# Kernel tuning notes

Measured on AMD Instinct MI355X. Metric: run time of the kernel, lower is better.

The kernel has to match this reference:

```python
import jax, jax.numpy as jnp
import numpy as np

HID, HEADS, EXP = 1024, 16, 4
HEAD_DIM = HID // HEADS
EPS = 1e-5


def setup_inputs() -> dict:
    key = jax.random.key(0)
    ks = jax.random.split(key, 16)
    s = 1.0 / np.sqrt(HID)
    d = dict(
        x=jax.random.normal(ks[0], (4, 2048, HID), jnp.float32),
        norm1_g=jnp.ones((HID,), jnp.float32),
        norm1_b=jnp.zeros((HID,), jnp.float32),
        wq=jax.random.normal(ks[1], (HID, HID), jnp.float32) * s,
        bq=jnp.zeros((HID,), jnp.float32),
        wk=jax.random.normal(ks[2], (HID, HID), jnp.float32) * s,
        bk=jnp.zeros((HID,), jnp.float32),
        wv=jax.random.normal(ks[3], (HID, HID), jnp.float32) * s,
        bv=jnp.zeros((HID,), jnp.float32),
        wo=jax.random.normal(ks[4], (HID, HID), jnp.float32) * s,
        bo=jnp.zeros((HID,), jnp.float32),
        norm2_g=jnp.ones((HID,), jnp.float32),
        norm2_b=jnp.zeros((HID,), jnp.float32),
        w1=jax.random.normal(ks[5], (HID * EXP, HID), jnp.float32) * s,
        b1=jnp.zeros((HID * EXP,), jnp.float32),
        w2=jax.random.normal(ks[6], (HID, HID * EXP), jnp.float32) * (1.0 / np.sqrt(HID * EXP)),
        b2=jnp.zeros((HID,), jnp.float32),
    )
    return d


def _layernorm(x, g, b):
    mu = jnp.mean(x, axis=-1, keepdims=True)
    var = jnp.mean(jnp.square(x - mu), axis=-1, keepdims=True)
    return (x - mu) * jax.lax.rsqrt(var + EPS) * g + b


def reference(x, norm1_g, norm1_b, wq, bq, wk, bk, wv, bv, wo, bo,
              norm2_g, norm2_b, w1, b1, w2, b2):
    B, S, _ = x.shape
    h = _layernorm(x, norm1_g, norm1_b)
    q = (h @ wq.T + bq).reshape(B, S, HEADS, HEAD_DIM)
    k = (h @ wk.T + bk).reshape(B, S, HEADS, HEAD_DIM)
    v = (h @ wv.T + bv).reshape(B, S, HEADS, HEAD_DIM)
    # scores: [B, H, S, S] (materialized, matching the naive original)
    scores = jnp.einsum('bshd,bthd->bhst', q, k) / np.sqrt(HEAD_DIM)
    attn = jax.nn.softmax(scores, axis=-1)
    out = jnp.einsum('bhst,bthd->bshd', attn, v).reshape(B, S, HID)
    x = x + out @ wo.T + bo
    h = _layernorm(x, norm2_g, norm2_b)
    ffn = jax.nn.relu(h @ w1.T + b1) @ w2.T + b2
    return x + ffn
```

## Files before the change

kernel.cpp:

```cpp
#include <hip/hip_runtime.h>
#include <hip/hip_bf16.h>

#define HID   1024
#define S_LEN 2048
#define NB    4
#define M_TOK 8192
#define HEADS 16
#define DH    64
#define FFN   4096

typedef __attribute__((ext_vector_type(8))) __bf16 bf16x8;
typedef __attribute__((ext_vector_type(4))) __bf16 bf16x4;
typedef __attribute__((ext_vector_type(4))) float  f32x4;

__device__ __forceinline__ void gl_lds16(const void* g, void* l) {
  __builtin_amdgcn_global_load_lds(
      (const __attribute__((address_space(1))) void*)g,
      (__attribute__((address_space(3))) void*)l, 16, 0, 0);
}

__device__ __forceinline__ int k3f(int r) { return (r ^ (r >> 3)) & 7; }

__global__ __launch_bounds__(256)
void cast_all_kernel(const float* __restrict__ a, const float* __restrict__ b,
                     const float* __restrict__ c, const float* __restrict__ d,
                     const float* __restrict__ e, const float* __restrict__ f,
                     __bf16* __restrict__ oa, __bf16* __restrict__ ob,
                     __bf16* __restrict__ oc, __bf16* __restrict__ od,
                     __bf16* __restrict__ oe, __bf16* __restrict__ og) {
  const int blk = blockIdx.x;
  const float* src; __bf16* dst; int boff;
  if (blk < 4096) {
    const int r = blk >> 10;
    src = (r == 0) ? a : (r == 1) ? b : (r == 2) ? c : d;
    dst = (r == 0) ? oa : (r == 1) ? ob : (r == 2) ? oc : od;
    boff = blk & 1023;
  } else if (blk < 8192) { src = e; dst = oe; boff = blk - 4096; }
  else                   { src = f; dst = og; boff = blk - 8192; }
  const int i = boff * 256 + threadIdx.x;
  float4 v = reinterpret_cast<const float4*>(src)[i];
  bf16x4 o = { (__bf16)v.x, (__bf16)v.y, (__bf16)v.z, (__bf16)v.w };
  reinterpret_cast<bf16x4*>(dst)[i] = o;
}

__global__ __launch_bounds__(256)
void ln_kernel(const float* __restrict__ x, const float* __restrict__ g,
               const float* __restrict__ bb, __bf16* __restrict__ out) {
  const int row = blockIdx.x;
  const int tid = threadIdx.x;
  const float4 v = reinterpret_cast<const float4*>(x + (size_t)row * HID)[tid];
  float s  = v.x + v.y + v.z + v.w;
  float sq = v.x*v.x + v.y*v.y + v.z*v.z + v.w*v.w;
  #pragma unroll
  for (int o = 32; o > 0; o >>= 1) { s += __shfl_down(s, o); sq += __shfl_down(sq, o); }
  __shared__ float ls[4], lq[4];
  if ((tid & 63) == 0) { ls[tid >> 6] = s; lq[tid >> 6] = sq; }
  __syncthreads();
  s  = ls[0] + ls[1] + ls[2] + ls[3];
  sq = lq[0] + lq[1] + lq[2] + lq[3];
  const float mu   = s * (1.0f / HID);
  const float rstd = rsqrtf(sq * (1.0f / HID) - mu * mu + 1e-5f);
  const float4 gv = reinterpret_cast<const float4*>(g)[tid];
  const float4 bv = reinterpret_cast<const float4*>(bb)[tid];
  bf16x4 o;
  o[0] = (__bf16)((v.x - mu) * rstd * gv.x + bv.x);
  o[1] = (__bf16)((v.y - mu) * rstd * gv.y + bv.y);
  o[2] = (__bf16)((v.z - mu) * rstd * gv.z + bv.z);
  o[3] = (__bf16)((v.w - mu) * rstd * gv.w + bv.w);
  reinterpret_cast<bf16x4*>(out + (size_t)row * HID)[tid] = o;
}

template<int EPI>
__global__ __launch_bounds__(256)
void gemm_bt(const __bf16* __restrict__ A, const __bf16* __restrict__ Bw,
             const float* __restrict__ bias, const float* __restrict__ res,
             __bf16* __restrict__ obf, float* __restrict__ of,
             int M, int N, int K) {
  __shared__ __bf16 Al[128 * 64];
  __shared__ __bf16 Bl[128 * 64];
  const int tid  = threadIdx.x;
  const int lane = tid & 63;
  const int wid  = tid >> 6;
  const int wm = wid >> 1, wn = wid & 1;
  const int nwg = gridDim.x * gridDim.y;
  const int bid = blockIdx.y * gridDim.x + blockIdx.x;
  const int swz = (bid & 7) * (nwg >> 3) + (bid >> 3);
  const long bm = (long)(swz / gridDim.x) * 128;
  const long bn = (long)(swz % gridDim.x) * 128;
  const int r8 = lane >> 3, c8 = lane & 7;

  f32x4 acc[4][4] = {};

  const int nk = K >> 6;
  for (int kt = 0; kt < nk; ++kt) {
    const int k0 = kt << 6;
    __syncthreads();
    #pragma unroll
    for (int i = 0; i < 4; ++i) {
      const int rbase = i * 32 + wid * 8;
      gl_lds16(A + (bm + rbase + r8) * (long)K + k0 + c8 * 8, &Al[rbase * 64]);
    }
    #pragma unroll
    for (int i = 0; i < 4; ++i) {
      const int rbase = i * 32 + wid * 8;
      gl_lds16(Bw + (bn + rbase + r8) * (long)K + k0 + c8 * 8, &Bl[rbase * 64]);
    }
    __syncthreads();
    #pragma unroll
    for (int kk = 0; kk < 2; ++kk) {
      bf16x8 af[4], bfr[4];
      #pragma unroll
      for (int mt = 0; mt < 4; ++mt)
        af[mt] = *(const bf16x8*)&Al[(wm * 64 + mt * 16 + (lane & 15)) * 64 + kk * 32 + (lane >> 4) * 8];
      #pragma unroll
      for (int nt = 0; nt < 4; ++nt)
        bfr[nt] = *(const bf16x8*)&Bl[(wn * 64 + nt * 16 + (lane & 15)) * 64 + kk * 32 + (lane >> 4) * 8];
      #pragma unroll
      for (int mt = 0; mt < 4; ++mt)
        #pragma unroll
        for (int nt = 0; nt < 4; ++nt)
          acc[mt][nt] = __builtin_amdgcn_mfma_f32_16x16x32_bf16(af[mt], bfr[nt], acc[mt][nt], 0, 0, 0);
    }
  }

  #pragma unroll
  for (int mt = 0; mt < 4; ++mt) {
    const long row0 = bm + wm * 64 + mt * 16 + ((lane >> 4) << 2);
    #pragma unroll
    for (int nt = 0; nt < 4; ++nt) {
      const long col = bn + wn * 64 + nt * 16 + (lane & 15);
      const float bsv = bias[col];
      #pragma unroll
      for (int j = 0; j < 4; ++j) {
        const float val = acc[mt][nt][j] + bsv;
        const long idx = (row0 + j) * (long)N + col;
        if (EPI == 2) of[idx] = res[idx] + val;
        else          obf[idx] = (__bf16)val;
      }
    }
  }
}

template<int EPI>
__global__ __launch_bounds__(512, 2)
void gemm_bt256(const __bf16* __restrict__ A, const __bf16* __restrict__ Bw,
                const float* __restrict__ bias,
                __bf16* __restrict__ obf, __bf16* __restrict__ ob2,
                __bf16* __restrict__ ob3, int M, int N, int K) {
  __shared__ __bf16 Al[2][256 * 64];
  __shared__ __bf16 Bl[2][256 * 64];
  const int tid  = threadIdx.x;
  const int lane = tid & 63;
  const int wid  = tid >> 6;
  const int wm = wid >> 2, wn = wid & 3;
  const int q15 = lane & 15, hi = lane >> 4;
  const int nwg = gridDim.x * gridDim.y;
  const int bid = blockIdx.y * gridDim.x + blockIdx.x;
  const int swz = (bid & 7) * (nwg >> 3) + (bid >> 3);
  const long bm = (long)(swz / gridDim.x) * 256;
  const long bn = (long)(swz % gridDim.x) * 256;
  const int sr = lane >> 3, sc = lane & 7;

  f32x4 acc[8][4] = {};
  const int nk = K >> 6;

  auto stage = [&](int b, int kt) {
    const long k0 = (long)kt << 6;
    #pragma unroll
    for (int p = 0; p < 4; ++p) {
      const int row = p * 64 + wid * 8 + sr;
      gl_lds16(A + (bm + row) * (long)K + k0 + ((sc ^ k3f(row)) << 3),
               &Al[b][(p * 64 + wid * 8) * 64]);
    }
    #pragma unroll
    for (int p = 0; p < 4; ++p) {
      const int row = p * 64 + wid * 8 + sr;
      gl_lds16(Bw + (bn + row) * (long)K + k0 + ((sc ^ k3f(row)) << 3),
               &Bl[b][(p * 64 + wid * 8) * 64]);
    }
  };

  stage(0, 0);
  int cur = 0;
  for (int t = 0; t < nk; ++t) {
    __builtin_amdgcn_s_barrier();
    __builtin_amdgcn_sched_barrier(0);
    if (t + 1 < nk) {
      stage(cur ^ 1, t + 1);
      __builtin_amdgcn_sched_barrier(0);
      asm volatile("s_waitcnt vmcnt(8)" ::: "memory");
    } else {
      asm volatile("s_waitcnt vmcnt(0)" ::: "memory");
    }
    __builtin_amdgcn_sched_barrier(0);
    __builtin_amdgcn_s_barrier();
    __builtin_amdgcn_sched_barrier(0);

    const __bf16* Ab = Al[cur];
    const __bf16* Bb = Bl[cur];
    #pragma unroll
    for (int kk = 0; kk < 2; ++kk) {
      bf16x8 af[8], bfr[4];
      #pragma unroll
      for (int mt = 0; mt < 8; ++mt) {
        const int row = wm * 128 + mt * 16 + q15;
        af[mt] = *(const bf16x8*)&Ab[row * 64 + (((kk * 4 + hi) ^ k3f(row)) << 3)];
      }
      #pragma unroll
      for (int nt = 0; nt < 4; ++nt) {
        const int row = wn * 64 + nt * 16 + q15;
        bfr[nt] = *(const bf16x8*)&Bb[row * 64 + (((kk * 4 + hi) ^ k3f(row)) << 3)];
      }
      __builtin_amdgcn_s_setprio(1);
      #pragma unroll
      for (int mt = 0; mt < 8; ++mt)
        #pragma unroll
        for (int nt = 0; nt < 4; ++nt)
          acc[mt][nt] = __builtin_amdgcn_mfma_f32_16x16x32_bf16(af[mt], bfr[nt], acc[mt][nt], 0, 0, 0);
      __builtin_amdgcn_s_setprio(0);
    }
    cur ^= 1;
  }

  #pragma unroll
  for (int mt = 0; mt < 8; ++mt) {
    const long row0 = bm + wm * 128 + mt * 16 + (hi << 2);
    #pragma unroll
    for (int nt = 0; nt < 4; ++nt) {
      const long col = bn + wn * 64 + nt * 16 + q15;
      const float bsv = bias[col];
      #pragma unroll
      for (int j = 0; j < 4; ++j) {
        const float val = acc[mt][nt][j] + bsv;
        if (EPI == 1) {
          obf[(row0 + j) * (long)N + col] = (__bf16)fmaxf(val, 0.0f);
        } else {
          __bf16* dst = (col < 1024) ? obf : ((col < 2048) ? ob2 : ob3);
          dst[(row0 + j) * 1024L + (col & 1023)] = (__bf16)val;
        }
      }
    }
  }
}

__global__ __launch_bounds__(256)
void vtrans_kernel(const __bf16* __restrict__ v, __bf16* __restrict__ vt) {
  __shared__ __bf16 t[4096];
  const int tid = threadIdx.x;
  const int bh = blockIdx.y, b = bh >> 4, h = bh & 15;
  const int s0 = blockIdx.x * 64;
  const int r = tid >> 3, c8 = tid & 7;
  #pragma unroll
  for (int i = 0; i < 2; ++i) {
    const int row = i * 32 + r;
    bf16x8 val = *(const bf16x8*)(v + ((size_t)(b * S_LEN + s0 + row)) * HID + h * DH + c8 * 8);
    *(bf16x8*)&t[row * 64 + ((c8 ^ k3f(row)) << 3)] = val;
  }
  __syncthreads();
  #pragma unroll
  for (int i = 0; i < 2; ++i) {
    const int d = i * 32 + r;
    bf16x8 ovec;
    #pragma unroll
    for (int j = 0; j < 8; ++j) {
      const int s = c8 * 8 + j;
      ovec[j] = t[s * 64 + ((((d >> 3) ^ k3f(s)) << 3) | (d & 7))];
    }
    *(bf16x8*)(vt + ((size_t)(bh * 64 + d)) * S_LEN + s0 + c8 * 8) = ovec;
  }
}

__global__ __launch_bounds__(256)
void attn_kernel(const __bf16* __restrict__ q, const __bf16* __restrict__ k,
                 const __bf16* __restrict__ vt, __bf16* __restrict__ o) {
  __shared__ __bf16 Kl[64 * 64];
  __shared__ __bf16 Vt[64 * 64];
  __shared__ __bf16 Pl[4 * 16 * 72];
  const int tid = threadIdx.x, lane = tid & 63, wid = tid >> 6;
  const int q15 = lane & 15, hi4 = lane >> 4;
  const int bh = blockIdx.x, b = bh >> 4, h = bh & 15;
  const size_t base = ((size_t)b * S_LEN) * HID + h * DH;
  const int q0 = blockIdx.y * 64 + wid * 16;
  const int r8 = lane >> 3, c8 = lane & 7;
  const __bf16* vth = vt + (size_t)bh * 64 * S_LEN;

  bf16x8 qf[2];
  {
    const __bf16* qp = q + base + (size_t)(q0 + q15) * HID + hi4 * 8;
    #pragma unroll
    for (int kk = 0; kk < 2; ++kk) {
      bf16x8 t = *(const bf16x8*)(qp + kk * 32);
      #pragma unroll
      for (int j = 0; j < 8; ++j) t[j] = (__bf16)((float)t[j] * 0.1803368801f);
      qf[kk] = t;
    }
  }

  f32x4 oacc[4] = {};
  float lp = 0.f;
  __bf16* pb = &Pl[wid * (16 * 72)];

  for (int kv0 = 0; kv0 < S_LEN; kv0 += 64) {
    __syncthreads();
    #pragma unroll
    for (int i = 0; i < 2; ++i) {
      const int rbase = i * 32 + wid * 8;
      const int row = rbase + r8;
      gl_lds16(k + base + (size_t)(kv0 + row) * HID + ((c8 ^ k3f(row)) << 3), &Kl[rbase * 64]);
    }
    #pragma unroll
    for (int i = 0; i < 2; ++i) {
      const int rbase = i * 32 + wid * 8;
      const int row = rbase + r8;
      gl_lds16(vth + (size_t)row * S_LEN + kv0 + ((c8 ^ k3f(row)) << 3), &Vt[rbase * 64]);
    }
    __syncthreads();

    f32x4 sacc[4] = {};
    __builtin_amdgcn_s_setprio(1);
    #pragma unroll
    for (int ct = 0; ct < 4; ++ct) {
      const int rk = ct * 16 + q15;
      const int k3 = k3f(rk);
      #pragma unroll
      for (int kk = 0; kk < 2; ++kk) {
        bf16x8 kf = *(const bf16x8*)&Kl[rk * 64 + (((kk * 4 + hi4) ^ k3) << 3)];
        sacc[ct] = __builtin_amdgcn_mfma_f32_16x16x32_bf16(kf, qf[kk], sacc[ct], 0, 0, 0);
      }
    }
    __builtin_amdgcn_s_setprio(0);

    #pragma unroll
    for (int ct = 0; ct < 4; ++ct) {
      bf16x4 w;
      #pragma unroll
      for (int jj = 0; jj < 4; ++jj) {
        const float p = exp2f(sacc[ct][jj] - 16.0f);
        lp += p;
        w[jj] = (__bf16)p;
      }
      *(bf16x4*)&pb[q15 * 72 + ct * 16 + hi4 * 4] = w;
    }

    __builtin_amdgcn_s_setprio(1);
    #pragma unroll
    for (int kk = 0; kk < 2; ++kk) {
      bf16x8 pf = *(const bf16x8*)&pb[q15 * 72 + kk * 32 + hi4 * 8];
      #pragma unroll
      for (int dt = 0; dt < 4; ++dt) {
        const int dv = dt * 16 + q15;
        bf16x8 vf = *(const bf16x8*)&Vt[dv * 64 + (((kk * 4 + hi4) ^ k3f(dv)) << 3)];
        oacc[dt] = __builtin_amdgcn_mfma_f32_16x16x32_bf16(pf, vf, oacc[dt], 0, 0, 0);
      }
    }
    __builtin_amdgcn_s_setprio(0);
  }

  float lrun = lp;
  lrun += __shfl_xor(lrun, 16);
  lrun += __shfl_xor(lrun, 32);
  const float inv = 1.0f / lrun;
  #pragma unroll
  for (int jj = 0; jj < 4; ++jj) {
    const float iO = __shfl(inv, (hi4 << 4) | (hi4 * 4 + jj));
    const size_t orow = base + (size_t)(q0 + hi4 * 4 + jj) * HID;
    #pragma unroll
    for (int dt = 0; dt < 4; ++dt)
      o[orow + dt * 16 + q15] = (__bf16)(oacc[dt][jj] * iO);
  }
}

extern "C" void kernel_launch(void* const* d_in, const int* in_sizes, int n_in,
                              void* d_out, int out_size, void* d_ws, size_t ws_size,
                              hipStream_t stream) {
  (void)in_sizes; (void)n_in; (void)out_size; (void)ws_size;
  const float* x   = (const float*)d_in[0];
  const float* n1g = (const float*)d_in[1];
  const float* n1b = (const float*)d_in[2];
  const float* wq  = (const float*)d_in[3];
  const float* bq  = (const float*)d_in[4];
  const float* wk  = (const float*)d_in[5];
  const float* bk  = (const float*)d_in[6];
  const float* wv  = (const float*)d_in[7];
  const float* bv  = (const float*)d_in[8];
  const float* wo  = (const float*)d_in[9];
  const float* bo  = (const float*)d_in[10];
  const float* n2g = (const float*)d_in[11];
  const float* n2b = (const float*)d_in[12];
  const float* w1  = (const float*)d_in[13];
  const float* b1  = (const float*)d_in[14];
  const float* w2  = (const float*)d_in[15];
  const float* b2  = (const float*)d_in[16];

  char* ws = (char*)d_ws;
  const size_t MB = 1ull << 20;
  __bf16* wq_b = (__bf16*)(ws);
  __bf16* wk_b = (__bf16*)(ws + 2 * MB);
  __bf16* wv_b = (__bf16*)(ws + 4 * MB);
  __bf16* wo_b = (__bf16*)(ws + 6 * MB);
  __bf16* w1_b = (__bf16*)(ws + 8 * MB);
  __bf16* w2_b = (__bf16*)(ws + 16 * MB);
  __bf16* h1   = (__bf16*)(ws + 24 * MB);
  __bf16* qb   = (__bf16*)(ws + 40 * MB);
  __bf16* kb   = (__bf16*)(ws + 56 * MB);
  __bf16* vb   = (__bf16*)(ws + 72 * MB);
  __bf16* vtb  = (__bf16*)(ws + 88 * MB);
  __bf16* ffn1 = (__bf16*)(ws + 56 * MB);
  float*  bqkv = (float*)(ws + 118 * MB);
  float*  x2   = (float*)(ws + 120 * MB);

  cast_all_kernel<<<12288, 256, 0, stream>>>(wq, wk, wv, wo, w1, w2,
                                             wq_b, wk_b, wv_b, wo_b, w1_b, w2_b);

  hipMemcpyAsync(bqkv,        bq, 1024 * sizeof(float), hipMemcpyDeviceToDevice, stream);
  hipMemcpyAsync(bqkv + 1024, bk, 1024 * sizeof(float), hipMemcpyDeviceToDevice, stream);
  hipMemcpyAsync(bqkv + 2048, bv, 1024 * sizeof(float), hipMemcpyDeviceToDevice, stream);

  ln_kernel<<<M_TOK, 256, 0, stream>>>(x, n1g, n1b, h1);

  dim3 gqkv(3072 / 256, M_TOK / 256);
  gemm_bt256<3><<<gqkv, 512, 0, stream>>>(h1, wq_b, bqkv, qb, kb, vb,
                                          M_TOK, 3072, HID);

  dim3 gt(S_LEN / 64, NB * HEADS);
  vtrans_kernel<<<gt, 256, 0, stream>>>(vb, vtb);

  dim3 ga(NB * HEADS, S_LEN / 64);
  attn_kernel<<<ga, 256, 0, stream>>>(qb, kb, vtb, h1);

  dim3 g1(HID / 128, M_TOK / 128);
  gemm_bt<2><<<g1, 256, 0, stream>>>(h1, wo_b, bo, x, nullptr, x2,
                                     M_TOK, HID, HID);

  ln_kernel<<<M_TOK, 256, 0, stream>>>(x2, n2g, n2b, qb);

  dim3 g2(FFN / 256, M_TOK / 256);
  gemm_bt256<1><<<g2, 512, 0, stream>>>(qb, w1_b, b1, ffn1, nullptr, nullptr,
                                        M_TOK, FFN, HID);

  gemm_bt<2><<<g1, 256, 0, stream>>>(ffn1, w2_b, b2, x2, nullptr, (float*)d_out,
                                     M_TOK, HID, FFN);
}
```

Before: 463.1 us.

## Replace 128x128 residual GEMM with double-buffered swizzled 256x128 tile kernel

The two residual-epilogue GEMMs (output projection and FFN down-projection) now use a new 512-thread kernel with a 256x128 tile. It double-buffers LDS so the next K-slice's global-to-LDS loads overlap the current MFMAs, XOR-swizzles the LDS layout to avoid bank conflicts, and raises wave priority around the MFMA block. The aim is to hide memory latency and reduce stalls at the syncthreads barriers of the old single-buffer kernel, at the cost of more LDS per block (96KB) and fewer blocks in the grid (256 workgroups).

```diff
diff --git a/kernel.cpp b/kernel.cpp
--- a/kernel.cpp
+++ b/kernel.cpp
@@ -71,77 +71,6 @@
 }
 
 template<int EPI>
-__global__ __launch_bounds__(256)
-void gemm_bt(const __bf16* __restrict__ A, const __bf16* __restrict__ Bw,
-             const float* __restrict__ bias, const float* __restrict__ res,
-             __bf16* __restrict__ obf, float* __restrict__ of,
-             int M, int N, int K) {
-  __shared__ __bf16 Al[128 * 64];
-  __shared__ __bf16 Bl[128 * 64];
-  const int tid  = threadIdx.x;
-  const int lane = tid & 63;
-  const int wid  = tid >> 6;
-  const int wm = wid >> 1, wn = wid & 1;
-  const int nwg = gridDim.x * gridDim.y;
-  const int bid = blockIdx.y * gridDim.x + blockIdx.x;
-  const int swz = (bid & 7) * (nwg >> 3) + (bid >> 3);
-  const long bm = (long)(swz / gridDim.x) * 128;
-  const long bn = (long)(swz % gridDim.x) * 128;
-  const int r8 = lane >> 3, c8 = lane & 7;
-
-  f32x4 acc[4][4] = {};
-
-  const int nk = K >> 6;
-  for (int kt = 0; kt < nk; ++kt) {
-    const int k0 = kt << 6;
-    __syncthreads();
-    #pragma unroll
-    for (int i = 0; i < 4; ++i) {
-      const int rbase = i * 32 + wid * 8;
-      gl_lds16(A + (bm + rbase + r8) * (long)K + k0 + c8 * 8, &Al[rbase * 64]);
-    }
-    #pragma unroll
-    for (int i = 0; i < 4; ++i) {
-      const int rbase = i * 32 + wid * 8;
-      gl_lds16(Bw + (bn + rbase + r8) * (long)K + k0 + c8 * 8, &Bl[rbase * 64]);
-    }
-    __syncthreads();
-    #pragma unroll
-    for (int kk = 0; kk < 2; ++kk) {
-      bf16x8 af[4], bfr[4];
-      #pragma unroll
-      for (int mt = 0; mt < 4; ++mt)
-        af[mt] = *(const bf16x8*)&Al[(wm * 64 + mt * 16 + (lane & 15)) * 64 + kk * 32 + (lane >> 4) * 8];
-      #pragma unroll
-      for (int nt = 0; nt < 4; ++nt)
-        bfr[nt] = *(const bf16x8*)&Bl[(wn * 64 + nt * 16 + (lane & 15)) * 64 + kk * 32 + (lane >> 4) * 8];
-      #pragma unroll
-      for (int mt = 0; mt < 4; ++mt)
-        #pragma unroll
-        for (int nt = 0; nt < 4; ++nt)
-          acc[mt][nt] = __builtin_amdgcn_mfma_f32_16x16x32_bf16(af[mt], bfr[nt], acc[mt][nt], 0, 0, 0);
-    }
-  }
-
-  #pragma unroll
-  for (int mt = 0; mt < 4; ++mt) {
-    const long row0 = bm + wm * 64 + mt * 16 + ((lane >> 4) << 2);
-    #pragma unroll
-    for (int nt = 0; nt < 4; ++nt) {
-      const long col = bn + wn * 64 + nt * 16 + (lane & 15);
-      const float bsv = bias[col];
-      #pragma unroll
-      for (int j = 0; j < 4; ++j) {
-        const float val = acc[mt][nt][j] + bsv;
-        const long idx = (row0 + j) * (long)N + col;
-        if (EPI == 2) of[idx] = res[idx] + val;
-        else          obf[idx] = (__bf16)val;
-      }
-    }
-  }
-}
-
-template<int EPI>
 __global__ __launch_bounds__(512, 2)
 void gemm_bt256(const __bf16* __restrict__ A, const __bf16* __restrict__ Bw,
                 const float* __restrict__ bias,
@@ -238,6 +167,101 @@
           __bf16* dst = (col < 1024) ? obf : ((col < 2048) ? ob2 : ob3);
           dst[(row0 + j) * 1024L + (col & 1023)] = (__bf16)val;
         }
+      }
+    }
+  }
+}
+
+__global__ __launch_bounds__(512, 2)
+void gemm_btMN(const __bf16* __restrict__ A, const __bf16* __restrict__ Bw,
+               const float* __restrict__ bias, const float* __restrict__ res,
+               float* __restrict__ of, int M, int N, int K) {
+  __shared__ __bf16 Al[2][256 * 64];
+  __shared__ __bf16 Bl[2][128 * 64];
+  const int tid  = threadIdx.x;
+  const int lane = tid & 63;
+  const int wid  = tid >> 6;
+  const int wm = wid >> 1, wn = wid & 1;
+  const int q15 = lane & 15, hi = lane >> 4;
+  const int nwg = gridDim.x * gridDim.y;
+  const int bid = blockIdx.y * gridDim.x + blockIdx.x;
+  const int swz = (bid & 7) * (nwg >> 3) + (bid >> 3);
+  const long bm = (long)(swz / gridDim.x) * 256;
+  const long bn = (long)(swz % gridDim.x) * 128;
+  const int sr = lane >> 3, sc = lane & 7;
+
+  f32x4 acc[4][4] = {};
+  const int nk = K >> 6;
+
+  auto stage = [&](int b, int kt) {
+    const long k0 = (long)kt << 6;
+    #pragma unroll
+    for (int p = 0; p < 4; ++p) {
+      const int row = wid * 32 + p * 8 + sr;
+      gl_lds16(A + (bm + row) * (long)K + k0 + ((sc ^ k3f(row)) << 3),
+               &Al[b][(wid * 32 + p * 8) * 64]);
+    }
+    #pragma unroll
+    for (int p = 0; p < 2; ++p) {
+      const int row = wid * 16 + p * 8 + sr;
+      gl_lds16(Bw + (bn + row) * (long)K + k0 + ((sc ^ k3f(row)) << 3),
+               &Bl[b][(wid * 16 + p * 8) * 64]);
+    }
+  };
+
+  stage(0, 0);
+  int cur = 0;
+  for (int t = 0; t < nk; ++t) {
+    __builtin_amdgcn_s_barrier();
+    __builtin_amdgcn_sched_barrier(0);
+    if (t + 1 < nk) {
+      stage(cur ^ 1, t + 1);
+      __builtin_amdgcn_sched_barrier(0);
+      asm volatile("s_waitcnt vmcnt(6)" ::: "memory");
+    } else {
+      asm volatile("s_waitcnt vmcnt(0)" ::: "memory");
+    }
+    __builtin_amdgcn_sched_barrier(0);
+    __builtin_amdgcn_s_barrier();
+    __builtin_amdgcn_sched_barrier(0);
+
+    const __bf16* Ab = Al[cur];
+    const __bf16* Bb = Bl[cur];
+    #pragma unroll
+    for (int kk = 0; kk < 2; ++kk) {
+      bf16x8 af[4], bfr[4];
+      #pragma unroll
+      for (int mt = 0; mt < 4; ++mt) {
+        const int row = wm * 64 + mt * 16 + q15;
+        af[mt] = *(const bf16x8*)&Ab[row * 64 + (((kk * 4 + hi) ^ k3f(row)) << 3)];
+      }
+      #pragma unroll
+      for (int nt = 0; nt < 4; ++nt) {
+        const int row = wn * 64 + nt * 16 + q15;
+        bfr[nt] = *(const bf16x8*)&Bb[row * 64 + (((kk * 4 + hi) ^ k3f(row)) << 3)];
+      }
+      __builtin_amdgcn_s_setprio(1);
+      #pragma unroll
+      for (int mt = 0; mt < 4; ++mt)
+        #pragma unroll
+        for (int nt = 0; nt < 4; ++nt)
+          acc[mt][nt] = __builtin_amdgcn_mfma_f32_16x16x32_bf16(af[mt], bfr[nt], acc[mt][nt], 0, 0, 0);
+      __builtin_amdgcn_s_setprio(0);
+    }
+    cur ^= 1;
+  }
+
+  #pragma unroll
+  for (int mt = 0; mt < 4; ++mt) {
+    const long row0 = bm + wm * 64 + mt * 16 + (hi << 2);
+    #pragma unroll
+    for (int nt = 0; nt < 4; ++nt) {
+      const long col = bn + wn * 64 + nt * 16 + q15;
+      const float bsv = bias[col];
+      #pragma unroll
+      for (int j = 0; j < 4; ++j) {
+        const long idx = (row0 + j) * (long)N + col;
+        of[idx] = res[idx] + acc[mt][nt][j] + bsv;
       }
     }
   }
@@ -428,9 +452,8 @@
   dim3 ga(NB * HEADS, S_LEN / 64);
   attn_kernel<<<ga, 256, 0, stream>>>(qb, kb, vtb, h1);
 
-  dim3 g1(HID / 128, M_TOK / 128);
-  gemm_bt<2><<<g1, 256, 0, stream>>>(h1, wo_b, bo, x, nullptr, x2,
-                                     M_TOK, HID, HID);
+  dim3 g1(HID / 128, M_TOK / 256);
+  gemm_btMN<<<g1, 512, 0, stream>>>(h1, wo_b, bo, x, x2, M_TOK, HID, HID);
 
   ln_kernel<<<M_TOK, 256, 0, stream>>>(x2, n2g, n2b, qb);
 
@@ -438,6 +461,6 @@
   gemm_bt256<1><<<g2, 512, 0, stream>>>(qb, w1_b, b1, ffn1, nullptr, nullptr,
                                         M_TOK, FFN, HID);
 
-  gemm_bt<2><<<g1, 256, 0, stream>>>(ffn1, w2_b, b2, x2, nullptr, (float*)d_out,
-                                     M_TOK, HID, FFN);
-}
+  gemm_btMN<<<g1, 512, 0, stream>>>(ffn1, w2_b, b2, x2, (float*)d_out,
+                                    M_TOK, HID, FFN);
+}
```

Result: no change. 454.4 us, median of 2 (-1.9%).
